# Performance work log

Hardware: AMD Instinct MI355X
Metric: run time of the kernel (lower is better)

Reference implementation:

```python
import jax, jax.numpy as jnp
import numpy as np

NUM_CLASSES = 16
IOU_TH = 0.5
SCORE_TH = 0.05
MAX_DET = 100
MAX_PER_CLASS = 100


def setup_inputs() -> dict:
    key = jax.random.key(0)
    kxy, kwh, kc, ks = jax.random.split(key, 4)
    B, N = 4, 2048
    # xyxy boxes inside a ~640x640 image
    xy = jax.random.uniform(kxy, (B, N, 2), dtype=jnp.float32) * 576.0
    wh = jax.random.uniform(kwh, (B, N, 2), dtype=jnp.float32) * 56.0 + 8.0
    cls = jax.random.randint(kc, (B, N), 0, NUM_CLASSES).astype(jnp.float32)
    score = jax.random.uniform(ks, (B, N), dtype=jnp.float32)
    predictions = jnp.concatenate(
        [xy, xy + wh, cls[..., None], score[..., None]], axis=-1
    )  # [B, N, 6] = (x1, y1, x2, y2, class, confidence)
    return {"predictions": predictions}


def _pairwise_iou(b):
    # b: [N, 4] in yxyx
    y1, x1, y2, x2 = b[:, 0], b[:, 1], b[:, 2], b[:, 3]
    area = (y2 - y1) * (x2 - x1)
    ih = jnp.clip(jnp.minimum(y2[:, None], y2[None, :]) - jnp.maximum(y1[:, None], y1[None, :]), 0.0)
    iw = jnp.clip(jnp.minimum(x2[:, None], x2[None, :]) - jnp.maximum(x1[:, None], x1[None, :]), 0.0)
    inter = ih * iw
    union = area[:, None] + area[None, :] - inter
    return jnp.where(inter > 0.0, inter / jnp.maximum(union, 1e-8), 0.0)


def _per_image(boxes, cls_id, score):
    # boxes: [N, 4] yxyx, cls_id: [N] int32, score: [N]
    N = boxes.shape[0]
    iou = _pairwise_iou(boxes)  # [N, N], shared across classes
    idx_r = jnp.arange(N)

    def per_class(c):
        # one-hot scoring: only boxes labelled c have nonzero score for class c
        sc = jnp.where(cls_id == c, score, 0.0)
        order = jnp.argsort(-sc)
        s = sc[order]
        b = boxes[order]
        iou_s = iou[order][:, order]
        valid = s > SCORE_TH

        def body(i, keep):
            sup = (iou_s[i] > IOU_TH) & (idx_r > i)
            return jnp.where(keep[i], keep & ~sup, keep)

        keep = jax.lax.fori_loop(0, N, body, valid)  # greedy suppression
        masked = jnp.where(keep, s, -1.0)
        top_s, top_i = jax.lax.top_k(masked, MAX_PER_CLASS)
        vmask = top_s > SCORE_TH
        return b[top_i], jnp.where(vmask, top_s, 0.0), vmask

    cb, cs, cv = jax.lax.map(per_class, jnp.arange(NUM_CLASSES))
    cb = cb.reshape(-1, 4)
    cs = cs.reshape(-1)
    cv = cv.reshape(-1)
    ccls = jnp.repeat(jnp.arange(NUM_CLASSES, dtype=jnp.float32), MAX_PER_CLASS)
    # merge per-class detections, keep global top MAX_DET by score
    top_s, top_i = jax.lax.top_k(jnp.where(cv, cs, -1.0), MAX_DET)
    vmask = top_s > SCORE_TH
    out_b = jnp.where(vmask[:, None], cb[top_i], 0.0)
    out_c = jnp.where(vmask, ccls[top_i], 0.0)
    out_s = jnp.where(vmask, top_s, 0.0)
    return out_b, out_c, out_s, jnp.sum(vmask.astype(jnp.int32))


def reference(predictions):
    # convert xyxy -> yxyx (pure coordinate permutation)
    boxes_yxyx = predictions[..., :4][..., jnp.array([1, 0, 3, 2])]
    cls_id = predictions[..., 4].astype(jnp.int32)
    score = predictions[..., 5]
    ob, oc, os, nvalid = jax.vmap(_per_image)(boxes_yxyx, cls_id, score)
    # convert kept boxes back yxyx -> xyxy, re-attach class and confidence.
    # Original layer returns a ragged tensor; we return the padded equivalent
    # [B, MAX_DET, 6] plus per-image valid counts (the ragged row lengths).
    ob_xyxy = ob[..., jnp.array([1, 0, 3, 2])]
    out = jnp.concatenate([ob_xyxy, oc[..., None], os[..., None]], axis=-1)
    return out, nvalid
```

## Files before the change

kernel.cpp:

```cpp
#include <hip/hip_runtime.h>

#define NMS_NUM_CLASSES 16
#define NMS_N 2048
#define NMS_IOU_TH 0.5f
#define NMS_SCORE_TH 0.05f
#define NMS_MAX_DET 100
#define NMS_MAX_PER_CLASS 100
#define NMS_NS (NMS_NUM_CLASSES * NMS_MAX_PER_CLASS)
#define NMS_TILE 192


__device__ __forceinline__ int nms_cmp(float sj, int ij, float sq, int iq) {
    return ((int)(sj > sq)) | (((int)(sj == sq)) & ((int)(ij < iq)));
}

__global__ __launch_bounds__(1024) void nms_per_class_kernel(
    const float* __restrict__ pred,
    float* __restrict__ ws_scores,
    float* __restrict__ ws_boxes,
    float* __restrict__ out,
    int B)
{
    const int b = blockIdx.x / NMS_NUM_CLASSES;
    const int c = blockIdx.x % NMS_NUM_CLASSES;
    const float* p = pred + (size_t)b * NMS_N * 6;
    const int tid = threadIdx.x;
    const int lane = tid & 63;
    const int w = tid >> 6;

    if (c == 0) {
        float* ob = out + (size_t)b * NMS_MAX_DET * 6;
        for (int t = tid; t < NMS_MAX_DET * 6; t += 1024) ob[t] = 0.0f;
        if (tid == 0) out[(size_t)B * NMS_MAX_DET * 6 + b] = 0.0f;
    }

    __shared__ float s_scu[NMS_N];
    __shared__ int   s_ixu[NMS_N];
    __shared__ float s_bxu[NMS_N * 4];
    __shared__ int   s_rk[NMS_N];
    __shared__ float s_sc[NMS_N];
    __shared__ float s_bx[NMS_N * 4];
    __shared__ unsigned char s_keep[NMS_N];
    __shared__ unsigned int s_supc[6 * NMS_TILE];
    __shared__ int s_m;

    if (tid == 0) s_m = 0;
    __syncthreads();

    const float2* p2 = (const float2*)p;
    for (int i = tid; i < NMS_N; i += 1024) {
        s_rk[i] = 0;
        float2 v0 = p2[i * 3 + 0];
        float2 v1 = p2[i * 3 + 1];
        float2 v2 = p2[i * 3 + 2];
        const bool ok = ((int)v2.x == c) && (v2.y > NMS_SCORE_TH);
        unsigned long long mask = __ballot(ok);
        int base = 0;
        if (lane == 0) {
            int cnt = __popcll(mask);
            if (cnt) base = atomicAdd(&s_m, cnt);
        }
        base = __shfl(base, 0, 64);
        if (ok) {
            int pos = base + __popcll(mask & ((1ull << lane) - 1ull));
            s_scu[pos] = v2.y;
            s_ixu[pos] = i;
            s_bxu[pos * 4 + 0] = v0.x;
            s_bxu[pos * 4 + 1] = v0.y;
            s_bxu[pos * 4 + 2] = v1.x;
            s_bxu[pos * 4 + 3] = v1.y;
        }
    }
    __syncthreads();
    const int M = s_m;

    {
        const int nch = (M + 31) >> 5;
        const int ntask = M * nch;
        for (int task = tid; task < ntask; task += 1024) {
            const int q = task % M;
            const int ch = task / M;
            const float sq = s_scu[q];
            const int   iq = s_ixu[q];
            const int j0 = ch << 5;
            int jend = j0 + 32; if (jend > M) jend = M;
            int r0 = 0, r1 = 0, r2 = 0, r3 = 0;
            int j = j0;
            for (; j + 4 <= jend; j += 4) {
                float sa = s_scu[j + 0], sb = s_scu[j + 1];
                float sc2 = s_scu[j + 2], sd = s_scu[j + 3];
                int ia = s_ixu[j + 0], ib = s_ixu[j + 1];
                int ic = s_ixu[j + 2], id = s_ixu[j + 3];
                r0 += nms_cmp(sa, ia, sq, iq);
                r1 += nms_cmp(sb, ib, sq, iq);
                r2 += nms_cmp(sc2, ic, sq, iq);
                r3 += nms_cmp(sd, id, sq, iq);
            }
            for (; j < jend; ++j)
                r0 += nms_cmp(s_scu[j], s_ixu[j], sq, iq);
            const int rk = (r0 + r1) + (r2 + r3);
            if (rk) atomicAdd(&s_rk[q], rk);
        }
    }
    __syncthreads();
    for (int q = tid; q < M; q += 1024) {
        int rk = s_rk[q];
        s_sc[rk] = s_scu[q];
        s_bx[rk * 4 + 0] = s_bxu[q * 4 + 0];
        s_bx[rk * 4 + 1] = s_bxu[q * 4 + 1];
        s_bx[rk * 4 + 2] = s_bxu[q * 4 + 2];
        s_bx[rk * 4 + 3] = s_bxu[q * 4 + 3];
        s_keep[rk] = 1;
    }
    __syncthreads();

    for (int t0 = 0; t0 < M; t0 += NMS_TILE) {
        const int tm = (M - t0 < NMS_TILE) ? (M - t0) : NMS_TILE;

        if (t0 > 0) {
            for (int jj = tid; jj < tm; jj += 1024) {
                const int gj = t0 + jj;
                float jx1 = s_bx[gj * 4 + 0], jy1 = s_bx[gj * 4 + 1];
                float jx2 = s_bx[gj * 4 + 2], jy2 = s_bx[gj * 4 + 3];
                float aj = (jy2 - jy1) * (jx2 - jx1);
                int dead = 0;
                for (int i = 0; i < t0 && !dead; ++i) {
                    if (!s_keep[i]) continue;
                    float ix1 = s_bx[i * 4 + 0], iy1 = s_bx[i * 4 + 1];
                    float ix2 = s_bx[i * 4 + 2], iy2 = s_bx[i * 4 + 3];
                    float ai = (iy2 - iy1) * (ix2 - ix1);
                    float ih = fminf(iy2, jy2) - fmaxf(iy1, jy1);
                    ih = fmaxf(ih, 0.0f);
                    float iw = fminf(ix2, jx2) - fmaxf(ix1, jx1);
                    iw = fmaxf(iw, 0.0f);
                    float inter = ih * iw;
                    float uni = ai + aj - inter;
                    float iou = (inter > 0.0f) ? inter / fmaxf(uni, 1e-08f) : 0.0f;
                    dead = iou > NMS_IOU_TH;
                }
                if (dead) s_keep[gj] = 0;
            }
            __syncthreads();
        }

        for (int idx = tid; idx < 6 * tm; idx += 1024) {
            const int wi = idx / tm;
            const int jj = idx % tm;
            const int ibase = wi << 5;
            unsigned int m0 = 0, m1 = 0, m2 = 0, m3 = 0;
            int iend = jj - ibase;
            if (iend > 32) iend = 32;
            if (iend > 0) {
                const int gj = t0 + jj;
                float jx1 = s_bx[gj * 4 + 0], jy1 = s_bx[gj * 4 + 1];
                float jx2 = s_bx[gj * 4 + 2], jy2 = s_bx[gj * 4 + 3];
                float aj = (jy2 - jy1) * (jx2 - jx1);
                int bb = 0;
                for (; bb + 4 <= iend; bb += 4) {
#define NMS_SUP1(K, MK)                                                        \
                    {                                                          \
                        const int gi = t0 + ibase + bb + (K);                  \
                        float ix1 = s_bx[gi * 4 + 0], iy1 = s_bx[gi * 4 + 1];  \
                        float ix2 = s_bx[gi * 4 + 2], iy2 = s_bx[gi * 4 + 3];  \
                        float ai = (iy2 - iy1) * (ix2 - ix1);                  \
                        float ih = fminf(iy2, jy2) - fmaxf(iy1, jy1);          \
                        ih = fmaxf(ih, 0.0f);                                  \
                        float iw = fminf(ix2, jx2) - fmaxf(ix1, jx1);          \
                        iw = fmaxf(iw, 0.0f);                                  \
                        float inter = ih * iw;                                 \
                        float uni = ai + aj - inter;                           \
                        float iou = (inter > 0.0f) ? inter / fmaxf(uni, 1e-08f) : 0.0f; \
                        MK |= (iou > NMS_IOU_TH) ? (1u << (bb + (K))) : 0u;    \
                    }
                    NMS_SUP1(0, m0)
                    NMS_SUP1(1, m1)
                    NMS_SUP1(2, m2)
                    NMS_SUP1(3, m3)
                }
                for (; bb < iend; ++bb) {
                    const int gi = t0 + ibase + bb;
                    float ix1 = s_bx[gi * 4 + 0], iy1 = s_bx[gi * 4 + 1];
                    float ix2 = s_bx[gi * 4 + 2], iy2 = s_bx[gi * 4 + 3];
                    float ai = (iy2 - iy1) * (ix2 - ix1);
                    float ih = fminf(iy2, jy2) - fmaxf(iy1, jy1);
                    ih = fmaxf(ih, 0.0f);
                    float iw = fminf(ix2, jx2) - fmaxf(ix1, jx1);
                    iw = fmaxf(iw, 0.0f);
                    float inter = ih * iw;
                    float uni = ai + aj - inter;
                    float iou = (inter > 0.0f) ? inter / fmaxf(uni, 1e-08f) : 0.0f;
                    m0 |= (iou > NMS_IOU_TH) ? (1u << bb) : 0u;
                }
#undef NMS_SUP1
            }
            s_supc[wi * NMS_TILE + jj] = (m0 | m1) | (m2 | m3);
        }
        __syncthreads();

        if (w == 0) {
            const int j0 = lane, j1 = lane + 64, j2 = lane + 128;
            const bool h0 = j0 < tm, h1 = j1 < tm, h2 = j2 < tm;
            unsigned int m00 = 0, m01 = 0, m02 = 0, m03 = 0, m04 = 0, m05 = 0;
            unsigned int m10 = 0, m11 = 0, m12 = 0, m13 = 0, m14 = 0, m15 = 0;
            unsigned int m20 = 0, m21 = 0, m22 = 0, m23 = 0, m24 = 0, m25 = 0;
            int ext0 = 0, ext1 = 0, ext2 = 0;
            if (h0) {
                m00 = s_supc[0 * NMS_TILE + j0];
                m01 = s_supc[1 * NMS_TILE + j0];
                m02 = s_supc[2 * NMS_TILE + j0];
                m03 = s_supc[3 * NMS_TILE + j0];
                m04 = s_supc[4 * NMS_TILE + j0];
                m05 = s_supc[5 * NMS_TILE + j0];
                ext0 = (int)s_keep[t0 + j0];
            }
            if (h1) {
                m10 = s_supc[0 * NMS_TILE + j1];
                m11 = s_supc[1 * NMS_TILE + j1];
                m12 = s_supc[2 * NMS_TILE + j1];
                m13 = s_supc[3 * NMS_TILE + j1];
                m14 = s_supc[4 * NMS_TILE + j1];
                m15 = s_supc[5 * NMS_TILE + j1];
                ext1 = (int)s_keep[t0 + j1];
            }
            if (h2) {
                m20 = s_supc[0 * NMS_TILE + j2];
                m21 = s_supc[1 * NMS_TILE + j2];
                m22 = s_supc[2 * NMS_TILE + j2];
                m23 = s_supc[3 * NMS_TILE + j2];
                m24 = s_supc[4 * NMS_TILE + j2];
                m25 = s_supc[5 * NMS_TILE + j2];
                ext2 = (int)s_keep[t0 + j2];
            }
            int alive0 = ext0, alive1 = ext1, alive2 = ext2;
            for (int round = 0; round < NMS_TILE; ++round) {
                unsigned long long A0b = __ballot(alive0 != 0);
                unsigned long long A1b = __ballot(alive1 != 0);
                unsigned long long A2b = __ballot(alive2 != 0);
                const unsigned int kw0 = (unsigned int)(A0b & 0xffffffffu);
                const unsigned int kw1 = (unsigned int)(A0b >> 32);
                const unsigned int kw2 = (unsigned int)(A1b & 0xffffffffu);
                const unsigned int kw3 = (unsigned int)(A1b >> 32);
                const unsigned int kw4 = (unsigned int)(A2b & 0xffffffffu);
                const unsigned int kw5 = (unsigned int)(A2b >> 32);
                int na0 = 0, na1 = 0, na2 = 0;
                if (ext0)
                    na0 = (((m00 & kw0) | (m01 & kw1) | (m02 & kw2) |
                            (m03 & kw3) | (m04 & kw4) | (m05 & kw5)) == 0u);
                if (ext1)
                    na1 = (((m10 & kw0) | (m11 & kw1) | (m12 & kw2) |
                            (m13 & kw3) | (m14 & kw4) | (m15 & kw5)) == 0u);
                if (ext2)
                    na2 = (((m20 & kw0) | (m21 & kw1) | (m22 & kw2) |
                            (m23 & kw3) | (m24 & kw4) | (m25 & kw5)) == 0u);
                const unsigned long long chg =
                    __ballot(na0 != alive0) | __ballot(na1 != alive1) |
                    __ballot(na2 != alive2);
                alive0 = na0; alive1 = na1; alive2 = na2;
                if (chg == 0ull) break;
            }
            if (h0) s_keep[t0 + j0] = (unsigned char)alive0;
            if (h1) s_keep[t0 + j1] = (unsigned char)alive1;
            if (h2) s_keep[t0 + j2] = (unsigned char)alive2;
        }
        __syncthreads();
    }

    if (w == 0) {
        const int chunk = (M + 63) >> 6;
        int lo = lane * chunk;
        int hi = lo + chunk; if (hi > M) hi = M;
        int cnt2 = 0;
        for (int jj = lo; jj < hi; ++jj) cnt2 += s_keep[jj];
        int inc2 = cnt2;
        for (int off = 1; off < 64; off <<= 1) {
            int n = __shfl_up(inc2, off, 64);
            if (lane >= off) inc2 += n;
        }
        int epos = inc2 - cnt2;
        const int total = __shfl(inc2, 63, 64);

        float* osc = ws_scores + ((size_t)b * NMS_NUM_CLASSES + c) * NMS_MAX_PER_CLASS;
        float* obx = ws_boxes + (((size_t)b * NMS_NUM_CLASSES + c) * NMS_MAX_PER_CLASS) * 4;
        for (int jj = lo; jj < hi; ++jj) {
            if (s_keep[jj]) {
                if (epos < NMS_MAX_PER_CLASS) {
                    osc[epos] = s_sc[jj];
                    obx[epos * 4 + 0] = s_bx[jj * 4 + 0];
                    obx[epos * 4 + 1] = s_bx[jj * 4 + 1];
                    obx[epos * 4 + 2] = s_bx[jj * 4 + 2];
                    obx[epos * 4 + 3] = s_bx[jj * 4 + 3];
                }
                epos++;
            }
        }
        for (int pp = lane; pp < NMS_MAX_PER_CLASS; pp += 64) {
            if (pp >= total) osc[pp] = -1.0f;
        }
    }
}

__global__ __launch_bounds__(1024) void nms_topk_kernel(
    const float* __restrict__ ws_scores,
    const float* __restrict__ ws_boxes,
    float* __restrict__ out,
    int B)
{
    const int b = blockIdx.x / NMS_NUM_CLASSES;
    const int c = blockIdx.x % NMS_NUM_CLASSES;
    const int cbase = c * NMS_MAX_PER_CLASS;
    __shared__ float s_sc[NMS_NS];
    __shared__ int s_rank[NMS_MAX_PER_CLASS];

    const float* isc = ws_scores + (size_t)b * NMS_NS;
    for (int t = threadIdx.x; t < NMS_NS; t += blockDim.x) s_sc[t] = isc[t];
    if (threadIdx.x < NMS_MAX_PER_CLASS) s_rank[threadIdx.x] = threadIdx.x;
    __syncthreads();

    {
        const int tA = threadIdx.x;
        const int tB = threadIdx.x + 1024;
        const bool hB = tB < NMS_MAX_PER_CLASS * 15;
        const int slotA = tA % NMS_MAX_PER_CLASS;
        const int chA0 = tA / NMS_MAX_PER_CLASS;
        const int chA = chA0 + (chA0 >= c ? 1 : 0);
        const int slotB = hB ? (tB % NMS_MAX_PER_CLASS) : slotA;
        const int chB0 = hB ? (tB / NMS_MAX_PER_CLASS) : chA0;
        const int chB = chB0 + (chB0 >= c ? 1 : 0);
        const int flatA = cbase + slotA;
        const int flatB = cbase + slotB;
        const float sA = s_sc[flatA];
        const float sB = s_sc[flatB];
        const int jA0 = chA * 100;
        const int jB0 = chB * 100;
        int a0 = 0, a1 = 0, a2 = 0, a3 = 0;
        int b0 = 0, b1 = 0, b2 = 0, b3 = 0;
        for (int k = 0; k < 100; k += 4) {
            const int ja = jA0 + k, jb = jB0 + k;
            float va0 = s_sc[ja + 0], va1 = s_sc[ja + 1];
            float va2 = s_sc[ja + 2], va3 = s_sc[ja + 3];
            float vb0 = s_sc[jb + 0], vb1 = s_sc[jb + 1];
            float vb2 = s_sc[jb + 2], vb3 = s_sc[jb + 3];
            a0 += ((int)(va0 > sA)) | (((int)(va0 == sA)) & ((int)(ja + 0 < flatA)));
            a1 += ((int)(va1 > sA)) | (((int)(va1 == sA)) & ((int)(ja + 1 < flatA)));
            a2 += ((int)(va2 > sA)) | (((int)(va2 == sA)) & ((int)(ja + 2 < flatA)));
            a3 += ((int)(va3 > sA)) | (((int)(va3 == sA)) & ((int)(ja + 3 < flatA)));
            b0 += ((int)(vb0 > sB)) | (((int)(vb0 == sB)) & ((int)(jb + 0 < flatB)));
            b1 += ((int)(vb1 > sB)) | (((int)(vb1 == sB)) & ((int)(jb + 1 < flatB)));
            b2 += ((int)(vb2 > sB)) | (((int)(vb2 == sB)) & ((int)(jb + 2 < flatB)));
            b3 += ((int)(vb3 > sB)) | (((int)(vb3 == sB)) & ((int)(jb + 3 < flatB)));
        }
        const int rkA = (a0 + a1) + (a2 + a3);
        const int rkB = (b0 + b1) + (b2 + b3);
        if (rkA) atomicAdd(&s_rank[slotA], rkA);
        if (hB && rkB) atomicAdd(&s_rank[slotB], rkB);
    }
    __syncthreads();

    int is_top = 0;
    const int t = threadIdx.x;
    if (t < NMS_MAX_PER_CLASS) {
        const int slot = cbase + t;
        float s = s_sc[slot];
        if (s > NMS_SCORE_TH) {
            int rk = s_rank[t];
            if (rk < NMS_MAX_DET) {
                const float* bx = ws_boxes + ((size_t)b * NMS_NS + slot) * 4;
                float* row = out + (size_t)b * NMS_MAX_DET * 6 + rk * 6;
                row[0] = bx[0];
                row[1] = bx[1];
                row[2] = bx[2];
                row[3] = bx[3];
                row[4] = (float)c;
                row[5] = s;
                is_top = 1;
            }
        }
    }
    unsigned long long m = __ballot(is_top);
    if ((threadIdx.x & 63) == 0) {
        float cnt = (float)__popcll(m);
        if (cnt > 0.0f)
            atomicAdd(&out[(size_t)B * NMS_MAX_DET * 6 + b], cnt);
    }
}

extern "C" void kernel_launch(void* const* d_in, const int* in_sizes, int n_in,
                              void* d_out, int out_size, void* d_ws, size_t ws_size,
                              hipStream_t stream) {
    const float* pred = (const float*)d_in[0];
    const int B = in_sizes[0] / (NMS_N * 6);
    if (B <= 0) return;
    float* out = (float*)d_out;

    float* ws_scores = (float*)d_ws;
    float* ws_boxes = ws_scores + (size_t)B * NMS_NS;

    nms_per_class_kernel<<<dim3(B * NMS_NUM_CLASSES), dim3(1024), 0, stream>>>(
        pred, ws_scores, ws_boxes, out, B);
    nms_topk_kernel<<<dim3(B * NMS_NUM_CLASSES), dim3(1024), 0, stream>>>(
        ws_scores, ws_boxes, out, B);
}
```

Measured before the change: 76.16 us.

## Fuse per-class NMS and global top-k via last-block-done counter

Merges the top-k merge kernel into the per-class NMS kernel. An atomic counter per image lets the last finishing class block do the global ranking. Ranking now uses binary search over each class's sorted score list instead of brute-force pairwise comparison. This removes one kernel launch and its gap, but adds a memset launch, and the final merge runs serially in one block per image.

```diff
diff --git a/kernel.cpp b/kernel.cpp
--- a/kernel.cpp
+++ b/kernel.cpp
@@ -14,10 +14,11 @@
     return ((int)(sj > sq)) | (((int)(sj == sq)) & ((int)(ij < iq)));
 }
 
-__global__ __launch_bounds__(1024) void nms_per_class_kernel(
+__global__ __launch_bounds__(1024) void nms_fused_kernel(
     const float* __restrict__ pred,
     float* __restrict__ ws_scores,
     float* __restrict__ ws_boxes,
+    int* __restrict__ ws_count,
     float* __restrict__ out,
     int B)
 {
@@ -28,12 +29,6 @@
     const int lane = tid & 63;
     const int w = tid >> 6;
 
-    if (c == 0) {
-        float* ob = out + (size_t)b * NMS_MAX_DET * 6;
-        for (int t = tid; t < NMS_MAX_DET * 6; t += 1024) ob[t] = 0.0f;
-        if (tid == 0) out[(size_t)B * NMS_MAX_DET * 6 + b] = 0.0f;
-    }
-
     __shared__ float s_scu[NMS_N];
     __shared__ int   s_ixu[NMS_N];
     __shared__ float s_bxu[NMS_N * 4];
@@ -43,6 +38,7 @@
     __shared__ unsigned char s_keep[NMS_N];
     __shared__ unsigned int s_supc[6 * NMS_TILE];
     __shared__ int s_m;
+    __shared__ int s_last;
 
     if (tid == 0) s_m = 0;
     __syncthreads();
@@ -297,91 +293,75 @@
             if (pp >= total) osc[pp] = -1.0f;
         }
     }
-}
-
-__global__ __launch_bounds__(1024) void nms_topk_kernel(
-    const float* __restrict__ ws_scores,
-    const float* __restrict__ ws_boxes,
-    float* __restrict__ out,
-    int B)
-{
-    const int b = blockIdx.x / NMS_NUM_CLASSES;
-    const int c = blockIdx.x % NMS_NUM_CLASSES;
-    const int cbase = c * NMS_MAX_PER_CLASS;
-    __shared__ float s_sc[NMS_NS];
-    __shared__ int s_rank[NMS_MAX_PER_CLASS];
+
+    __syncthreads();
+    __threadfence();
+    if (tid == 0) {
+        int old = atomicAdd(&ws_count[b], 1);
+        s_last = (old == NMS_NUM_CLASSES - 1);
+    }
+    __syncthreads();
+    if (!s_last) return;
+    __threadfence();
 
     const float* isc = ws_scores + (size_t)b * NMS_NS;
-    for (int t = threadIdx.x; t < NMS_NS; t += blockDim.x) s_sc[t] = isc[t];
-    if (threadIdx.x < NMS_MAX_PER_CLASS) s_rank[threadIdx.x] = threadIdx.x;
+    for (int t = tid; t < NMS_NS; t += 1024) s_scu[t] = isc[t];
+    float* ob = out + (size_t)b * NMS_MAX_DET * 6;
+    for (int t = tid; t < NMS_MAX_DET * 6; t += 1024) ob[t] = 0.0f;
+    if (tid == 0) s_m = 0;
+    __syncthreads();
+
+    for (int slot = tid; slot < NMS_NS; slot += 1024) {
+        const int c2 = slot / NMS_MAX_PER_CLASS;
+        const int i  = slot % NMS_MAX_PER_CLASS;
+        const float s = s_scu[slot];
+        int rk = i;
+        for (int cc = 0; cc < NMS_NUM_CLASSES; ++cc) {
+            if (cc == c2) continue;
+            const int base = cc * NMS_MAX_PER_CLASS;
+            int lo = 0, hi = NMS_MAX_PER_CLASS;
+            while (lo < hi) {
+                int mid = (lo + hi) >> 1;
+                if (s_scu[base + mid] > s) lo = mid + 1; else hi = mid;
+            }
+            int add = lo;
+            if (cc < c2) {
+                int lo2 = lo, hi2 = NMS_MAX_PER_CLASS;
+                while (lo2 < hi2) {
+                    int mid = (lo2 + hi2) >> 1;
+                    if (s_scu[base + mid] >= s) lo2 = mid + 1; else hi2 = mid;
+                }
+                add += (lo2 - lo);
+            }
+            rk += add;
+        }
+        s_rk[slot] = rk;
+    }
     __syncthreads();
 
     {
-        const int tA = threadIdx.x;
-        const int tB = threadIdx.x + 1024;
-        const bool hB = tB < NMS_MAX_PER_CLASS * 15;
-        const int slotA = tA % NMS_MAX_PER_CLASS;
-        const int chA0 = tA / NMS_MAX_PER_CLASS;
-        const int chA = chA0 + (chA0 >= c ? 1 : 0);
-        const int slotB = hB ? (tB % NMS_MAX_PER_CLASS) : slotA;
-        const int chB0 = hB ? (tB / NMS_MAX_PER_CLASS) : chA0;
-        const int chB = chB0 + (chB0 >= c ? 1 : 0);
-        const int flatA = cbase + slotA;
-        const int flatB = cbase + slotB;
-        const float sA = s_sc[flatA];
-        const float sB = s_sc[flatB];
-        const int jA0 = chA * 100;
-        const int jB0 = chB * 100;
-        int a0 = 0, a1 = 0, a2 = 0, a3 = 0;
-        int b0 = 0, b1 = 0, b2 = 0, b3 = 0;
-        for (int k = 0; k < 100; k += 4) {
-            const int ja = jA0 + k, jb = jB0 + k;
-            float va0 = s_sc[ja + 0], va1 = s_sc[ja + 1];
-            float va2 = s_sc[ja + 2], va3 = s_sc[ja + 3];
-            float vb0 = s_sc[jb + 0], vb1 = s_sc[jb + 1];
-            float vb2 = s_sc[jb + 2], vb3 = s_sc[jb + 3];
-            a0 += ((int)(va0 > sA)) | (((int)(va0 == sA)) & ((int)(ja + 0 < flatA)));
-            a1 += ((int)(va1 > sA)) | (((int)(va1 == sA)) & ((int)(ja + 1 < flatA)));
-            a2 += ((int)(va2 > sA)) | (((int)(va2 == sA)) & ((int)(ja + 2 < flatA)));
-            a3 += ((int)(va3 > sA)) | (((int)(va3 == sA)) & ((int)(ja + 3 < flatA)));
-            b0 += ((int)(vb0 > sB)) | (((int)(vb0 == sB)) & ((int)(jb + 0 < flatB)));
-            b1 += ((int)(vb1 > sB)) | (((int)(vb1 == sB)) & ((int)(jb + 1 < flatB)));
-            b2 += ((int)(vb2 > sB)) | (((int)(vb2 == sB)) & ((int)(jb + 2 < flatB)));
-            b3 += ((int)(vb3 > sB)) | (((int)(vb3 == sB)) & ((int)(jb + 3 < flatB)));
-        }
-        const int rkA = (a0 + a1) + (a2 + a3);
-        const int rkB = (b0 + b1) + (b2 + b3);
-        if (rkA) atomicAdd(&s_rank[slotA], rkA);
-        if (hB && rkB) atomicAdd(&s_rank[slotB], rkB);
-    }
-    __syncthreads();
-
-    int is_top = 0;
-    const int t = threadIdx.x;
-    if (t < NMS_MAX_PER_CLASS) {
-        const int slot = cbase + t;
-        float s = s_sc[slot];
-        if (s > NMS_SCORE_TH) {
-            int rk = s_rank[t];
-            if (rk < NMS_MAX_DET) {
-                const float* bx = ws_boxes + ((size_t)b * NMS_NS + slot) * 4;
-                float* row = out + (size_t)b * NMS_MAX_DET * 6 + rk * 6;
-                row[0] = bx[0];
-                row[1] = bx[1];
-                row[2] = bx[2];
-                row[3] = bx[3];
-                row[4] = (float)c;
-                row[5] = s;
-                is_top = 1;
-            }
-        }
-    }
-    unsigned long long m = __ballot(is_top);
-    if ((threadIdx.x & 63) == 0) {
-        float cnt = (float)__popcll(m);
-        if (cnt > 0.0f)
-            atomicAdd(&out[(size_t)B * NMS_MAX_DET * 6 + b], cnt);
-    }
+        int mycnt = 0;
+        for (int slot = tid; slot < NMS_NS; slot += 1024) {
+            const float s = s_scu[slot];
+            if (s > NMS_SCORE_TH) {
+                const int rk = s_rk[slot];
+                if (rk < NMS_MAX_DET) {
+                    const float* bx = ws_boxes + ((size_t)b * NMS_NS + slot) * 4;
+                    float* row = ob + rk * 6;
+                    row[0] = bx[0];
+                    row[1] = bx[1];
+                    row[2] = bx[2];
+                    row[3] = bx[3];
+                    row[4] = (float)(slot / NMS_MAX_PER_CLASS);
+                    row[5] = s;
+                    mycnt++;
+                }
+            }
+        }
+        if (mycnt) atomicAdd(&s_m, mycnt);
+    }
+    __syncthreads();
+    if (tid == 0) out[(size_t)B * NMS_MAX_DET * 6 + b] = (float)s_m;
 }
 
 extern "C" void kernel_launch(void* const* d_in, const int* in_sizes, int n_in,
@@ -393,10 +373,11 @@
     float* out = (float*)d_out;
 
     float* ws_scores = (float*)d_ws;
-    float* ws_boxes = ws_scores + (size_t)B * NMS_NS;
-
-    nms_per_class_kernel<<<dim3(B * NMS_NUM_CLASSES), dim3(1024), 0, stream>>>(
-        pred, ws_scores, ws_boxes, out, B);
-    nms_topk_kernel<<<dim3(B * NMS_NUM_CLASSES), dim3(1024), 0, stream>>>(
-        ws_scores, ws_boxes, out, B);
+    float* ws_boxes  = ws_scores + (size_t)B * NMS_NS;
+    int*   ws_count  = (int*)(ws_boxes + (size_t)B * NMS_NS * 4);
+
+    hipMemsetAsync(ws_count, 0, (size_t)B * sizeof(int), stream);
+
+    nms_fused_kernel<<<dim3(B * NMS_NUM_CLASSES), dim3(1024), 0, stream>>>(
+        pred, ws_scores, ws_boxes, ws_count, out, B);
 }
```

After: 112.9 us. 48.3% more time.
